# Performance work log

Measured on AMD Instinct MI355X. Metric: run time of the kernel, lower is better.

Reference implementation:

```python
import jax, jax.numpy as jnp
import numpy as np

REPEAT = 75  # upsample_repeat
UP = 4       # upsample_convs[0]


def setup_inputs() -> dict:
    key = jax.random.key(0)
    ks = jax.random.split(key, 12)
    B, L, F = 4, 48, 80
    C, H, A = 256, 896, 256  # conditional_size, rnn_size, signal_channels
    T = L * UP * REPEAT
    def xav(k, shape, fan_in):
        return jax.random.normal(k, shape, jnp.float32) * (1.0 / np.sqrt(fan_in))
    return {
        "local_features": jax.random.normal(ks[0], (B, L, F), jnp.float32),
        "gold_signal": jax.random.uniform(ks[1], (B, T), jnp.float32, -1.0, 1.0),
        "proj_w": xav(ks[2], (C, F), F),
        "proj_b": jnp.zeros((C,), jnp.float32),
        "up_w": xav(ks[3], (C, C, UP), C),
        "up_b": jnp.zeros((C,), jnp.float32),
        "embed_w": xav(ks[4], (C,), 1),
        "embed_b": jnp.zeros((C,), jnp.float32),
        "gru_wi": xav(ks[5], (3 * H, C), C),
        "gru_wh": xav(ks[6], (3 * H, H), H),
        "gru_bi": jnp.zeros((3 * H,), jnp.float32),
        "gru_bh": jnp.zeros((3 * H,), jnp.float32),
        "out_w1": xav(ks[7], (H, H), H),
        "out_b1": jnp.zeros((H,), jnp.float32),
        "out_w2": xav(ks[8], (A, H), H),
        "out_b2": jnp.zeros((A,), jnp.float32),
    }


def _forward(local_features, gold_signal, proj_w, proj_b, up_w, up_b,
             embed_w, embed_b, gru_wi, gru_wh, gru_bi, gru_bh,
             out_w1, out_b1, out_w2, out_b2):
    B = local_features.shape[0]
    O = up_w.shape[0]
    # --- conditional feature upsample ---
    # 1x1 conv: [B,L,F] -> [B,C,L]
    x = jnp.einsum("blf,cf->bcl", local_features, proj_w) + proj_b[None, :, None]
    # transposed conv, kernel=stride=UP: [B,C,L] -> [B,C,L*UP]
    x = jnp.einsum("bcl,ock->bolk", x, up_w).reshape(B, O, -1) + up_b[None, :, None]
    cond = jnp.repeat(x, REPEAT, axis=2)  # [B,C,T]
    # --- embed gold signal (1x1 conv, in_channels=1) ---
    sig = gold_signal[:, None, :] * embed_w[None, :, None] + embed_b[None, :, None]
    feats = (sig + cond).transpose(2, 0, 1)  # [T,B,C]
    # --- GRU (torch semantics), precompute input projections ---
    xp = feats @ gru_wi.T + gru_bi  # [T,B,3H]
    H = gru_wh.shape[1]

    def step(h, xpt):
        gh = h @ gru_wh.T + gru_bh
        xr, xz, xn = jnp.split(xpt, 3, axis=-1)
        hr, hz, hn = jnp.split(gh, 3, axis=-1)
        r = jax.nn.sigmoid(xr + hr)
        z = jax.nn.sigmoid(xz + hz)
        n = jnp.tanh(xn + r * hn)
        h_new = (1.0 - z) * n + z * h
        return h_new, h_new

    h0 = jnp.zeros((B, H), feats.dtype)
    _, hs = jax.lax.scan(step, h0, xp)  # [T,B,H]
    # --- output MLP + log-softmax over channels ---
    y = jax.nn.relu(hs @ out_w1.T + out_b1)
    logits = y @ out_w2.T + out_b2  # [T,B,A]
    logp = jax.nn.log_softmax(logits, axis=2)
    return logp.transpose(1, 2, 0)  # [B,A,T]


def reference(local_features, gold_signal, proj_w, proj_b, up_w, up_b,
              embed_w, embed_b, gru_wi, gru_wh, gru_bi, gru_bh,
              out_w1, out_b1, out_w2, out_b2):
    return _forward(local_features, gold_signal, proj_w, proj_b, up_w, up_b,
                    embed_w, embed_b, gru_wi, gru_wh, gru_bi, gru_bh,
                    out_w1, out_b1, out_w2, out_b2)
```

## Files before the change

kernel.cpp:

```cpp
#include <hip/hip_runtime.h>
#include <hip/hip_bf16.h>

#define B_ 4
#define L_ 48
#define F_ 80
#define C_ 256
#define H_ 896
#define G3_ 2688
#define A_ 256
#define T_ 14400
#define NBLK_ 192
#define REP_ 75

#define NMEM 28
#define RPW 12

typedef _Float16 __attribute__((ext_vector_type(8))) f16x8;
typedef __attribute__((ext_vector_type(4))) float f32x4;
typedef _Float16 __attribute__((ext_vector_type(2))) half2_;

__device__ __forceinline__ float fdot2f16(unsigned int a, unsigned int b, float c){
  return __builtin_amdgcn_fdot2(__builtin_bit_cast(half2_, a), __builtin_bit_cast(half2_, b), c, false);
}
__device__ __forceinline__ unsigned short f2h(float x){
  return __builtin_bit_cast(unsigned short, (_Float16)x);
}
__device__ __forceinline__ unsigned int packh2(float a, float b){
  return (unsigned int)f2h(a) | ((unsigned int)f2h(b) << 16);
}

template<int CTRL>
__device__ __forceinline__ float dppadd(float x){
  int r = __builtin_amdgcn_update_dpp(0, __builtin_bit_cast(int, x), CTRL, 0xF, 0xF, true);
  return x + __builtin_bit_cast(float, r);
}
__device__ __forceinline__ float wred(float x){
  x = dppadd<0xB1>(x);
  x = dppadd<0x4E>(x);
  x = dppadd<0x124>(x);
  x = dppadd<0x128>(x);
  x = dppadd<0x142>(x);
  x = dppadd<0x143>(x);
  return x;
}

__device__ __forceinline__ void ld7_llc(const unsigned int* base, unsigned int* hd){
  asm volatile(
    "global_load_dword %0, %7, off sc0 sc1\n\t"
    "global_load_dword %1, %7, off offset:256 sc0 sc1\n\t"
    "global_load_dword %2, %7, off offset:512 sc0 sc1\n\t"
    "global_load_dword %3, %7, off offset:768 sc0 sc1\n\t"
    "global_load_dword %4, %7, off offset:1024 sc0 sc1\n\t"
    "global_load_dword %5, %7, off offset:1280 sc0 sc1\n\t"
    "global_load_dword %6, %7, off offset:1536 sc0 sc1\n\t"
    "s_waitcnt vmcnt(0)"
    : "=&v"(hd[0]), "=&v"(hd[1]), "=&v"(hd[2]), "=&v"(hd[3]),
      "=&v"(hd[4]), "=&v"(hd[5]), "=&v"(hd[6])
    : "v"(base)
    : "memory");
}

__global__ void k_transpose_pw(const float* __restrict__ pw, float* __restrict__ pwT){
  int idx = blockIdx.x * 256 + threadIdx.x;
  if (idx >= F_ * C_) return;
  int f = idx / C_, c = idx % C_;
  pwT[idx] = pw[c * F_ + f];
}

__global__ void k_x1(const float* __restrict__ lf, const float* __restrict__ pwT,
                     const float* __restrict__ pb, float* __restrict__ x1){
  int bl = blockIdx.x;
  int c = threadIdx.x;
  const float* lrow = lf + (size_t)bl * F_;
  float acc = pb[c];
  for (int f = 0; f < F_; ++f) acc = fmaf(lrow[f], pwT[f * C_ + c], acc);
  x1[(size_t)bl * C_ + c] = acc;
}

__global__ void k_transpose_up(const float* __restrict__ up, float* __restrict__ upT){
  int idx = blockIdx.x * 256 + threadIdx.x;
  int o = idx % C_, c = (idx / C_) % C_, k = idx / (C_ * C_);
  upT[idx] = up[(o * C_ + c) * 4 + k];
}

__global__ void k_cond(const float* __restrict__ upT, const float* __restrict__ x1,
                       const float* __restrict__ ub, float* __restrict__ cond){
  int bblk = blockIdx.x;
  int blk = bblk % NBLK_;
  int b = bblk / NBLK_;
  int l = blk >> 2, kk = blk & 3;
  int o = threadIdx.x;
  const float* x1row = x1 + ((size_t)b * L_ + l) * C_;
  const float* uT = upT + (size_t)kk * C_ * C_;
  float acc = ub[o];
  for (int c = 0; c < C_; ++c) acc = fmaf(x1row[c], uT[c * C_ + o], acc);
  cond[(size_t)bblk * C_ + o] = acc;
}

__global__ void k_transpose_wi(const float* __restrict__ wi, float* __restrict__ wiT){
  int idx = blockIdx.x * 256 + threadIdx.x;
  int g = idx % G3_, c = idx / G3_;
  wiT[idx] = wi[(size_t)g * C_ + c];
}

__global__ void k_v(const float* __restrict__ wiT, const float* __restrict__ eb,
                    const float* __restrict__ cond, const float* __restrict__ bi,
                    float* __restrict__ v){
  int idx = blockIdx.x * 512 + threadIdx.x;
  int g = idx % G3_;
  int bblk = idx / G3_;
  const float* crow = cond + (size_t)bblk * C_;
  float acc = bi[g];
  for (int c = 0; c < C_; ++c) acc = fmaf(eb[c] + crow[c], wiT[(size_t)c * G3_ + g], acc);
  v[idx] = acc;
}

__global__ void k_u(const float* __restrict__ wiT, const float* __restrict__ ew,
                    float* __restrict__ u){
  int g = blockIdx.x * 256 + threadIdx.x;
  if (g >= G3_) return;
  float acc = 0.f;
  for (int c = 0; c < C_; ++c) acc = fmaf(ew[c], wiT[(size_t)c * G3_ + g], acc);
  u[g] = acc;
}

__global__ void k_packwh(const float* __restrict__ wh, unsigned int* __restrict__ whp){
  int idx = blockIdx.x * 256 + threadIdx.x;
  int lane = idx & 63;
  int r2 = idx >> 6;
  int dw = r2 % 7; int r3 = r2 / 7;
  int i = r3 % RPW; int W = r3 / RPW;
  int g = (i >> 2) * H_ + W * 4 + (i & 3);
  int k = dw * 128 + lane * 2;
  const float* p = wh + (size_t)g * H_ + k;
  whp[idx] = packh2(p[0], p[1]);
}

__global__ void k_cvth(const float* __restrict__ src, unsigned short* __restrict__ dst, int n){
  int idx = blockIdx.x * 256 + threadIdx.x;
  if (idx >= n) return;
  dst[idx] = f2h(src[idx]);
}

__global__ __launch_bounds__(576, 1) void k_gru(
    const float* __restrict__ gold, const float* __restrict__ v,
    const float* __restrict__ u, const float* __restrict__ bh,
    const unsigned int* __restrict__ whp,
    unsigned short* hsx)
{
  const int bid = blockIdx.x;
  const int batch = (bid & 7) >> 1;
  const int m = ((bid >> 3) << 1) | (bid & 1);
  const int tid = threadIdx.x;
  const int wave = tid >> 6;
  const int lane = tid & 63;

  __shared__ unsigned int lds_h[2][448];

  if (wave == 8){
    for (int t = 0; t < T_; ++t){
      const unsigned int* hp =
          (const unsigned int*)(hsx + ((size_t)t * B_ + batch) * H_) + lane;
      unsigned int hd[7];
      for (;;){
        ld7_llc(hp, hd);
        bool ok = (hd[0] != ~0u) & (hd[1] != ~0u) & (hd[2] != ~0u) &
                  (hd[3] != ~0u) & (hd[4] != ~0u) & (hd[5] != ~0u) & (hd[6] != ~0u);
        if (__all(ok)) break;
      }
#pragma unroll
      for (int dw = 0; dw < 7; ++dw) lds_h[t & 1][dw * 64 + lane] = hd[dw];
      __syncthreads();
    }
    return;
  }

  const int W = m * 8 + wave;

  unsigned int wreg[RPW][7];
#pragma unroll
  for (int i = 0; i < RPW; ++i){
    const unsigned int* p = whp + ((size_t)(W * RPW + i) * 7) * 64 + lane;
#pragma unroll
    for (int dw = 0; dw < 7; ++dw) wreg[i][dw] = p[dw * 64];
  }

  const bool owner = (lane >= 48) && (lane < 52);
  const int jj = lane - 48;
  const int jg = 4 * W + (jj & 3);
  float u3[3] = {0,0,0}, bh3[3] = {0,0,0}, v3[3] = {0,0,0}, v3n[3] = {0,0,0};
  float hcur = 0.f;
  if (owner){
    u3[0] = u[jg]; u3[1] = u[jg + H_]; u3[2] = u[jg + 2 * H_];
    bh3[0] = bh[jg]; bh3[1] = bh[jg + H_]; bh3[2] = bh[jg + 2 * H_];
    const float* vp = v + ((size_t)(batch * NBLK_)) * G3_ + jg;
    v3[0] = vp[0]; v3[1] = vp[H_]; v3[2] = vp[2 * H_];
  }
  const float* goldb = gold + (size_t)batch * T_;
  int cnt = 0, blkc = 0;

  for (int t = 0; t < T_; ++t){
    float go = goldb[t];
    __syncthreads();
    unsigned int hd[7];
#pragma unroll
    for (int dw = 0; dw < 7; ++dw) hd[dw] = lds_h[t & 1][dw * 64 + lane];

    float acc[RPW];
#pragma unroll
    for (int i = 0; i < RPW; ++i){
      float a = 0.f;
#pragma unroll
      for (int dw = 0; dw < 7; ++dw) a = fdot2f16(wreg[i][dw], hd[dw], a);
      acc[i] = wred(a);
    }

    if (owner){
      if (cnt == REP_ - 2){
        int nb = blkc + 1; if (nb > NBLK_ - 1) nb = NBLK_ - 1;
        const float* vp = v + ((size_t)(batch * NBLK_ + nb)) * G3_ + jg;
        v3n[0] = vp[0]; v3n[1] = vp[H_]; v3n[2] = vp[2 * H_];
      }
      float hr = jj==0 ? acc[0] : jj==1 ? acc[1] : jj==2 ? acc[2]  : acc[3];
      float hz = jj==0 ? acc[4] : jj==1 ? acc[5] : jj==2 ? acc[6]  : acc[7];
      float hn = jj==0 ? acc[8] : jj==1 ? acc[9] : jj==2 ? acc[10] : acc[11];
      hr += bh3[0]; hz += bh3[1]; hn += bh3[2];
      float xr = fmaf(go, u3[0], v3[0]);
      float xz = fmaf(go, u3[1], v3[1]);
      float xn = fmaf(go, u3[2], v3[2]);
      float r = 1.f / (1.f + __expf(-(xr + hr)));
      float z = 1.f / (1.f + __expf(-(xz + hz)));
      float e = __expf(2.f * (xn + r * hn));
      float n = 1.f - 2.f / (e + 1.f);
      float hnew = (1.f - z) * n + z * hcur;
      hcur = hnew;
      unsigned int h16 = (unsigned int)f2h(hnew);
      unsigned int oth = (unsigned int)__builtin_amdgcn_update_dpp(
          0, (int)h16, 0xB1, 0xF, 0xF, true);
      if ((jj & 1) == 0){
        unsigned int packed = h16 | (oth << 16);
        unsigned int* dst = (unsigned int*)(hsx + ((size_t)(t + 1) * B_ + batch) * H_)
                          + 2 * W + (jj >> 1);
        __hip_atomic_store(dst, packed, __ATOMIC_RELAXED, __HIP_MEMORY_SCOPE_AGENT);
      }
    }
    if (++cnt == REP_){
      cnt = 0; ++blkc;
      v3[0] = v3n[0]; v3[1] = v3n[1]; v3[2] = v3n[2];
    }
  }
}

__global__ __launch_bounds__(256) void k_mlp(
    const unsigned short* hs, const unsigned short* __restrict__ w1h,
    const unsigned short* __restrict__ w2h, const float* __restrict__ ob1,
    const float* __restrict__ ob2, float* logits)
{
  const int mtile = blockIdx.x * 32;
  const int tid = threadIdx.x;
  const int wid = tid >> 6, lane = tid & 63;
  const int l15 = lane & 15, l4 = lane >> 4;
  __shared__ unsigned short y_lds[32 * 904];

  for (int nblk = 0; nblk < 14; ++nblk){
    f32x4 acc[2] = {(f32x4)(0.f), (f32x4)(0.f)};
    const int colg = nblk * 64 + wid * 16 + l15;
    for (int kk = 0; kk < 28; ++kk){
      const int k = kk * 32 + l4 * 8;
      f16x8 bfrag = *(const f16x8*)(w1h + (size_t)colg * H_ + k);
#pragma unroll
      for (int mf = 0; mf < 2; ++mf){
        f16x8 afrag = *(const f16x8*)(hs + (size_t)(mtile + mf * 16 + l15) * H_ + k);
        acc[mf] = __builtin_amdgcn_mfma_f32_16x16x32_f16(afrag, bfrag, acc[mf], 0, 0, 0);
      }
    }
    float bias = ob1[colg];
#pragma unroll
    for (int mf = 0; mf < 2; ++mf)
#pragma unroll
      for (int rg = 0; rg < 4; ++rg){
        float yv = acc[mf][rg] + bias;
        yv = yv > 0.f ? yv : 0.f;
        y_lds[(mf * 16 + l4 * 4 + rg) * 904 + colg] = f2h(yv);
      }
  }
  __syncthreads();

  f32x4 a2acc[2][4];
#pragma unroll
  for (int mf = 0; mf < 2; ++mf)
#pragma unroll
    for (int nf = 0; nf < 4; ++nf) a2acc[mf][nf] = (f32x4)(0.f);

  for (int kk = 0; kk < 28; ++kk){
    const int k = kk * 32 + l4 * 8;
    f16x8 a2[2];
#pragma unroll
    for (int mf = 0; mf < 2; ++mf)
      a2[mf] = *(const f16x8*)(&y_lds[(mf * 16 + l15) * 904 + k]);
#pragma unroll
    for (int nf = 0; nf < 4; ++nf){
      const int col = wid * 64 + nf * 16 + l15;
      f16x8 bfrag = *(const f16x8*)(w2h + (size_t)col * H_ + k);
#pragma unroll
      for (int mf = 0; mf < 2; ++mf)
        a2acc[mf][nf] = __builtin_amdgcn_mfma_f32_16x16x32_f16(a2[mf], bfrag, a2acc[mf][nf], 0, 0, 0);
    }
  }
#pragma unroll
  for (int nf = 0; nf < 4; ++nf){
    const int col = wid * 64 + nf * 16 + l15;
    const float bias = ob2[col];
#pragma unroll
    for (int mf = 0; mf < 2; ++mf)
#pragma unroll
      for (int rg = 0; rg < 4; ++rg){
        const int mrow = mtile + mf * 16 + l4 * 4 + rg;
        logits[(size_t)mrow * 448 + col] = a2acc[mf][nf][rg] + bias;
      }
  }
}

__global__ __launch_bounds__(256) void k_softmax(const float* __restrict__ logits,
                                                 float* __restrict__ out)
{
  const int bid = blockIdx.x;
  const int b = bid / 225;
  const int t0 = (bid % 225) * 64;
  const int tid = threadIdx.x;
  __shared__ float pm[64][4];
  __shared__ float ps[64][4];
  __shared__ float lz[64];
  {
    const int r = tid >> 2, q = tid & 3;
    const float* row = logits + (size_t)((t0 + r) * 4 + b) * 448 + q * 64;
    float mx = -1e30f;
    for (int j = 0; j < 64; ++j) mx = fmaxf(mx, row[j]);
    float s = 0.f;
    for (int j = 0; j < 64; ++j) s += __expf(row[j] - mx);
    pm[r][q] = mx; ps[r][q] = s;
  }
  __syncthreads();
  if (tid < 64){
    float m0 = pm[tid][0], m1 = pm[tid][1], m2 = pm[tid][2], m3 = pm[tid][3];
    float mx = fmaxf(fmaxf(m0, m1), fmaxf(m2, m3));
    float s = ps[tid][0] * __expf(m0 - mx) + ps[tid][1] * __expf(m1 - mx)
            + ps[tid][2] * __expf(m2 - mx) + ps[tid][3] * __expf(m3 - mx);
    lz[tid] = mx + logf(s);
  }
  __syncthreads();
  for (int i = 0; i < 64; ++i){
    const int idx = i * 256 + tid;
    const int a = idx >> 6, tt = idx & 63;
    float x = logits[(size_t)((t0 + tt) * 4 + b) * 448 + a];
    out[((size_t)(b * A_) + a) * T_ + t0 + tt] = x - lz[tt];
  }
}

extern "C" void kernel_launch(void* const* d_in, const int* in_sizes, int n_in,
                              void* d_out, int out_size, void* d_ws, size_t ws_size,
                              hipStream_t stream)
{
  (void)in_sizes; (void)n_in; (void)out_size; (void)ws_size;
  const float* lf   = (const float*)d_in[0];
  const float* gold = (const float*)d_in[1];
  const float* pw   = (const float*)d_in[2];
  const float* pb   = (const float*)d_in[3];
  const float* upw  = (const float*)d_in[4];
  const float* upb  = (const float*)d_in[5];
  const float* ew   = (const float*)d_in[6];
  const float* eb   = (const float*)d_in[7];
  const float* wi   = (const float*)d_in[8];
  const float* wh   = (const float*)d_in[9];
  const float* bi   = (const float*)d_in[10];
  const float* bhp  = (const float*)d_in[11];
  const float* w1   = (const float*)d_in[12];
  const float* b1   = (const float*)d_in[13];
  const float* w2   = (const float*)d_in[14];
  const float* b2   = (const float*)d_in[15];
  float* out = (float*)d_out;
  char* ws = (char*)d_ws;

  size_t off = 0;
  auto take = [&](size_t bytes){
    size_t r = off; off += (bytes + 255) & ~(size_t)255; return r;
  };
  float* pwT  = (float*)(ws + take((size_t)F_ * C_ * 4));
  float* x1   = (float*)(ws + take((size_t)B_ * L_ * C_ * 4));
  float* upT  = (float*)(ws + take((size_t)4 * C_ * C_ * 4));
  float* cond = (float*)(ws + take((size_t)B_ * NBLK_ * C_ * 4));
  float* wiT  = (float*)(ws + take((size_t)C_ * G3_ * 4));
  float* v    = (float*)(ws + take((size_t)B_ * NBLK_ * G3_ * 4));
  float* u    = (float*)(ws + take((size_t)G3_ * 4));
  unsigned int*   whp = (unsigned int*)(ws + take((size_t)224 * RPW * 7 * 64 * 4));
  unsigned short* w1h = (unsigned short*)(ws + take((size_t)H_ * H_ * 2));
  unsigned short* w2h = (unsigned short*)(ws + take((size_t)A_ * H_ * 2));
  unsigned short* hsx = (unsigned short*)(ws + take((size_t)(T_ + 1) * B_ * H_ * 2));

  hipMemsetAsync((void*)hsx, 0, (size_t)B_ * H_ * 2, stream);
  hipMemsetAsync((void*)(hsx + (size_t)B_ * H_), 0xFF, (size_t)T_ * B_ * H_ * 2, stream);

  k_transpose_pw<<<80, 256, 0, stream>>>(pw, pwT);
  k_x1<<<B_ * L_, 256, 0, stream>>>(lf, pwT, pb, x1);
  k_transpose_up<<<1024, 256, 0, stream>>>(upw, upT);
  k_cond<<<B_ * NBLK_, 256, 0, stream>>>(upT, x1, upb, cond);
  k_transpose_wi<<<2688, 256, 0, stream>>>(wi, wiT);
  k_v<<<4032, 512, 0, stream>>>(wiT, eb, cond, bi, v);
  k_u<<<11, 256, 0, stream>>>(wiT, ew, u);
  k_packwh<<<4704, 256, 0, stream>>>(wh, whp);
  k_cvth<<<(H_ * H_ + 255) / 256, 256, 0, stream>>>(w1, w1h, H_ * H_);
  k_cvth<<<(A_ * H_ + 255) / 256, 256, 0, stream>>>(w2, w2h, A_ * H_);

  k_gru<<<112, 576, 0, stream>>>(gold, v, u, bhp, whp, hsx);

  const unsigned short* hs_mlp = hsx + (size_t)B_ * H_;
  float* logits = (float*)hsx + (size_t)B_ * 448;
  k_mlp<<<1800, 256, 0, stream>>>(hs_mlp, w1h, w2h, b1, b2, logits);
  k_softmax<<<900, 256, 0, stream>>>(logits, out);
}
```

Baseline: 36.38 ms.

## Add busy filler blocks to GRU grid and widen hidden-state stores to 64-bit

The GRU grid grows from 112 to 256 blocks. The extra 144 blocks spin on dependent FMAs until the final timestep's hidden state shows up in global memory. The apparent aim is to occupy the remaining CUs, possibly to hold clocks up or keep other work off the device, while the real blocks use large dynamic LDS so each block takes a full CU. Separately, each lane group now packs four fp16 hidden values with a DPP swizzle and writes one 64-bit atomic store instead of two 32-bit stores, halving the store count per step. Risks: the filler blocks draw power and may lower clocks, and the scheme assumes all 256 blocks are co-resident.

New measurement: 37.48 ms. +3.0%, slower.

```diff
diff --git a/kernel.cpp b/kernel.cpp
--- a/kernel.cpp
+++ b/kernel.cpp
@@ -14,6 +14,9 @@
 
 #define NMEM 28
 #define RPW 12
+#define NREAL 112
+#define GRU_GRID 256
+#define DYN_LDS 81920
 
 typedef _Float16 __attribute__((ext_vector_type(8))) f16x8;
 typedef __attribute__((ext_vector_type(4))) float f32x4;
@@ -148,14 +151,41 @@
     const unsigned int* __restrict__ whp,
     unsigned short* hsx)
 {
+  extern __shared__ unsigned int dynls[];
   const int bid = blockIdx.x;
-  const int batch = (bid & 7) >> 1;
-  const int m = ((bid >> 3) << 1) | (bid & 1);
   const int tid = threadIdx.x;
   const int wave = tid >> 6;
   const int lane = tid & 63;
 
-  __shared__ unsigned int lds_h[2][448];
+  if (bid >= NREAL){
+    volatile unsigned int* bflag = dynls;
+    if (tid == 0) dynls[0] = 0;
+    __syncthreads();
+    const unsigned int* slotT = (const unsigned int*)(hsx + ((size_t)T_ * B_) * H_);
+    float x = 1.0f + (float)tid * 1e-6f;
+    float a = 1.0000001f, b = 0.9999999f;
+    for (;;){
+#pragma unroll 64
+      for (int i = 0; i < 4096; ++i)
+        asm volatile("v_fmac_f32 %0, %1, %2" : "+v"(x) : "v"(a), "v"(b));
+      if (wave == 0){
+        unsigned int d = ~0u;
+        if (lane < 4){
+          const unsigned int* pp = slotT + lane * 448;
+          asm volatile("global_load_dword %0, %1, off sc0 sc1\n\ts_waitcnt vmcnt(0)"
+                       : "=v"(d) : "v"(pp) : "memory");
+        }
+        bool ok = (lane < 4) ? (d != ~0u) : true;
+        if (__all(ok) && lane == 0) *bflag = 1u;
+      }
+      if (*bflag) break;
+    }
+    return;
+  }
+
+  const int batch = (bid & 7) >> 1;
+  const int m = ((bid >> 3) << 1) | (bid & 1);
+  unsigned int (*lds_h)[448] = (unsigned int(*)[448])dynls;
 
   if (wave == 8){
     for (int t = 0; t < T_; ++t){
@@ -237,11 +267,16 @@
       unsigned int h16 = (unsigned int)f2h(hnew);
       unsigned int oth = (unsigned int)__builtin_amdgcn_update_dpp(
           0, (int)h16, 0xB1, 0xF, 0xF, true);
-      if ((jj & 1) == 0){
-        unsigned int packed = h16 | (oth << 16);
-        unsigned int* dst = (unsigned int*)(hsx + ((size_t)(t + 1) * B_ + batch) * H_)
-                          + 2 * W + (jj >> 1);
-        __hip_atomic_store(dst, packed, __ATOMIC_RELAXED, __HIP_MEMORY_SCOPE_AGENT);
+      unsigned int packed = h16 | (oth << 16);
+      unsigned int p23 = (unsigned int)__builtin_amdgcn_update_dpp(
+          0, (int)packed, 0x4E, 0xF, 0xF, true);
+      if (jj == 0){
+        unsigned long long v64 = (unsigned long long)packed
+                               | ((unsigned long long)p23 << 32);
+        unsigned long long* dst =
+            (unsigned long long*)((unsigned int*)(hsx + ((size_t)(t + 1) * B_ + batch) * H_)
+                                  + 2 * W);
+        __hip_atomic_store(dst, v64, __ATOMIC_RELAXED, __HIP_MEMORY_SCOPE_AGENT);
       }
     }
     if (++cnt == REP_){
@@ -397,6 +432,9 @@
   unsigned short* w2h = (unsigned short*)(ws + take((size_t)A_ * H_ * 2));
   unsigned short* hsx = (unsigned short*)(ws + take((size_t)(T_ + 1) * B_ * H_ * 2));
 
+  hipFuncSetAttribute((const void*)k_gru,
+                      hipFuncAttributeMaxDynamicSharedMemorySize, DYN_LDS);
+
   hipMemsetAsync((void*)hsx, 0, (size_t)B_ * H_ * 2, stream);
   hipMemsetAsync((void*)(hsx + (size_t)B_ * H_), 0xFF, (size_t)T_ * B_ * H_ * 2, stream);
 
@@ -411,7 +449,7 @@
   k_cvth<<<(H_ * H_ + 255) / 256, 256, 0, stream>>>(w1, w1h, H_ * H_);
   k_cvth<<<(A_ * H_ + 255) / 256, 256, 0, stream>>>(w2, w2h, A_ * H_);
 
-  k_gru<<<112, 576, 0, stream>>>(gold, v, u, bhp, whp, hsx);
+  k_gru<<<GRU_GRID, 576, DYN_LDS, stream>>>(gold, v, u, bhp, whp, hsx);
 
   const unsigned short* hs_mlp = hsx + (size_t)B_ * H_;
   float* logits = (float*)hsx + (size_t)B_ * 448;
```

## Replace per-step block barrier with per-chunk LDS flags and 64-bit hidden-state stores

Applied to the files above, without the earlier changes.

The poller wave now publishes each of the 7 hidden-state dword chunks to LDS as soon as that chunk is valid and raises a workgroup-scope flag for it. The compute waves spin on those flags instead of waiting at a __syncthreads every timestep, so their dot products can start on early chunks before the whole vector has arrived. The owner lanes also combine four fp16 outputs with DPP and write them as one 64-bit atomic store instead of two 32-bit stores. In exchange, compute waves busy-wait on LDS, and ordering now relies on relaxed atomics plus an explicit lgkmcnt wait rather than a barrier.

Measured after the change: 41.54 ms. +14.2%, slower.

```diff
diff --git a/kernel.cpp b/kernel.cpp
--- a/kernel.cpp
+++ b/kernel.cpp
@@ -156,21 +156,33 @@
   const int lane = tid & 63;
 
   __shared__ unsigned int lds_h[2][448];
+  __shared__ int flags[8];
+
+  if (tid < 8) flags[tid] = 0;
+  __syncthreads();
 
   if (wave == 8){
     for (int t = 0; t < T_; ++t){
       const unsigned int* hp =
           (const unsigned int*)(hsx + ((size_t)t * B_ + batch) * H_) + lane;
-      unsigned int hd[7];
-      for (;;){
+      unsigned int pend = 0x7F;
+      do {
+        unsigned int hd[7];
         ld7_llc(hp, hd);
-        bool ok = (hd[0] != ~0u) & (hd[1] != ~0u) & (hd[2] != ~0u) &
-                  (hd[3] != ~0u) & (hd[4] != ~0u) & (hd[5] != ~0u) & (hd[6] != ~0u);
-        if (__all(ok)) break;
-      }
-#pragma unroll
-      for (int dw = 0; dw < 7; ++dw) lds_h[t & 1][dw * 64 + lane] = hd[dw];
-      __syncthreads();
+#pragma unroll
+        for (int dw = 0; dw < 7; ++dw){
+          if (pend & (1u << dw)){
+            if (__all(hd[dw] != ~0u)){
+              lds_h[t & 1][dw * 64 + lane] = hd[dw];
+              asm volatile("s_waitcnt lgkmcnt(0)" ::: "memory");
+              if (lane == 0)
+                __hip_atomic_store(&flags[dw], t + 1, __ATOMIC_RELAXED,
+                                   __HIP_MEMORY_SCOPE_WORKGROUP);
+              pend &= ~(1u << dw);
+            }
+          }
+        }
+      } while (pend);
     }
     return;
   }
@@ -201,19 +213,22 @@
 
   for (int t = 0; t < T_; ++t){
     float go = goldb[t];
-    __syncthreads();
-    unsigned int hd[7];
-#pragma unroll
-    for (int dw = 0; dw < 7; ++dw) hd[dw] = lds_h[t & 1][dw * 64 + lane];
 
     float acc[RPW];
 #pragma unroll
-    for (int i = 0; i < RPW; ++i){
-      float a = 0.f;
-#pragma unroll
-      for (int dw = 0; dw < 7; ++dw) a = fdot2f16(wreg[i][dw], hd[dw], a);
-      acc[i] = wred(a);
-    }
+    for (int i = 0; i < RPW; ++i) acc[i] = 0.f;
+
+#pragma unroll
+    for (int dw = 0; dw < 7; ++dw){
+      while (__hip_atomic_load(&flags[dw], __ATOMIC_RELAXED,
+                               __HIP_MEMORY_SCOPE_WORKGROUP) < t + 1) {}
+      unsigned int hdw = lds_h[t & 1][dw * 64 + lane];
+#pragma unroll
+      for (int i = 0; i < RPW; ++i) acc[i] = fdot2f16(wreg[i][dw], hdw, acc[i]);
+    }
+
+#pragma unroll
+    for (int i = 0; i < RPW; ++i) acc[i] = wred(acc[i]);
 
     if (owner){
       if (cnt == REP_ - 2){
@@ -237,11 +252,16 @@
       unsigned int h16 = (unsigned int)f2h(hnew);
       unsigned int oth = (unsigned int)__builtin_amdgcn_update_dpp(
           0, (int)h16, 0xB1, 0xF, 0xF, true);
-      if ((jj & 1) == 0){
-        unsigned int packed = h16 | (oth << 16);
-        unsigned int* dst = (unsigned int*)(hsx + ((size_t)(t + 1) * B_ + batch) * H_)
-                          + 2 * W + (jj >> 1);
-        __hip_atomic_store(dst, packed, __ATOMIC_RELAXED, __HIP_MEMORY_SCOPE_AGENT);
+      unsigned int packed = h16 | (oth << 16);
+      unsigned int p23 = (unsigned int)__builtin_amdgcn_update_dpp(
+          0, (int)packed, 0x4E, 0xF, 0xF, true);
+      if (jj == 0){
+        unsigned long long v64 = (unsigned long long)packed
+                               | ((unsigned long long)p23 << 32);
+        unsigned long long* dst =
+            (unsigned long long*)((unsigned int*)(hsx + ((size_t)(t + 1) * B_ + batch) * H_)
+                                  + 2 * W);
+        __hip_atomic_store(dst, v64, __ATOMIC_RELAXED, __HIP_MEMORY_SCOPE_AGENT);
       }
     }
     if (++cnt == REP_){
```
